# Kernel optimization log

Hardware: AMD Instinct MI355X
Metric: run time of the kernel (lower is better)

The kernel has to match this reference:

```python
import jax, jax.numpy as jnp
import numpy as np

B, S, H = 64, 512, 768        # batch, seq_len, bert hidden
WE, ML, D = 4, 5, 50          # word_enhance_size, max_lexicon_length, word emb dim
V, T = 700000, 21             # lexicon vocab, num_labels


def setup_inputs() -> dict:
    key = jax.random.key(0)
    ks = jax.random.split(key, 10)
    return {
        "sequence_output": jax.random.normal(ks[0], (B, S, H), jnp.float32),
        "soft_lexicon_ids": jax.random.randint(ks[1], (B, S, WE, ML), 0, V),
        "soft_lexicon_weights": jax.random.uniform(ks[2], (B, S, WE, ML), jnp.float32),
        "label_ids": jax.random.randint(ks[3], (B, S), 0, T),
        "attention_mask": jnp.ones((B, S), jnp.int32),
        "word_emb": jax.random.normal(ks[4], (V, D), jnp.float32) * 0.02,
        "W": jax.random.normal(ks[5], (H + WE * D, T), jnp.float32) * 0.02,
        "b": jnp.zeros((T,), jnp.float32),
        "start_trans": jax.random.normal(ks[6], (T,), jnp.float32) * 0.1,
        "end_trans": jax.random.normal(ks[7], (T,), jnp.float32) * 0.1,
        "trans": jax.random.normal(ks[8], (T, T), jnp.float32) * 0.1,
    }


def _crf_nll(emissions, tags, mask, start_trans, end_trans, trans):
    """torchcrf-style CRF negative log-likelihood, reduction='sum'.
    emissions [B,S,T], tags [B,S] int, mask [B,S] in {0,1} (mask[:,0]==1)."""
    maskf = mask.astype(emissions.dtype)
    # ---- numerator: score of the gold path ----
    em_sc = jnp.take_along_axis(emissions, tags[..., None], axis=-1)[..., 0]  # [B,S]
    trans_sc = trans[tags[:, :-1], tags[:, 1:]]                               # [B,S-1]
    num = start_trans[tags[:, 0]] + em_sc[:, 0] \
        + jnp.sum((trans_sc + em_sc[:, 1:]) * maskf[:, 1:], axis=-1)
    last_idx = jnp.sum(mask, axis=-1).astype(jnp.int32) - 1
    last_tags = jnp.take_along_axis(tags, last_idx[:, None], axis=1)[:, 0]
    num = num + end_trans[last_tags]
    # ---- denominator: forward algorithm (logsumexp recursion) ----
    alpha0 = start_trans[None, :] + emissions[:, 0]          # [B,T]
    em_t = jnp.swapaxes(emissions[:, 1:], 0, 1)              # [S-1,B,T]
    mk_t = jnp.swapaxes(mask[:, 1:], 0, 1)                   # [S-1,B]

    def step(alpha, inp):
        e_t, m_t = inp
        nxt = jax.scipy.special.logsumexp(
            alpha[:, :, None] + trans[None, :, :] + e_t[:, None, :], axis=1)
        return jnp.where(m_t[:, None] > 0, nxt, alpha), None

    alpha, _ = jax.lax.scan(step, alpha0, (em_t, mk_t))
    logZ = jax.scipy.special.logsumexp(alpha + end_trans[None, :], axis=-1)
    return -jnp.sum(num - logZ)


def reference(sequence_output, soft_lexicon_ids, soft_lexicon_weights, label_ids,
              attention_mask, word_emb, W, b, start_trans, end_trans, trans):
    Bn, Sn = sequence_output.shape[0], sequence_output.shape[1]
    # soft-lexicon gather + weighted sum over matched words: [B,S,WE,ML,D] -> [B,S,WE,D]
    lex = word_emb[soft_lexicon_ids]                                   # gather
    lex = jnp.einsum('bswld,bswl->bswd', lex, soft_lexicon_weights)    # weight + reduce ML
    lex = lex.reshape(Bn, Sn, -1)                                      # [B,S,WE*D]
    feats = jnp.concatenate([sequence_output, lex], axis=-1)           # [B,S,H+WE*D]
    logits = feats @ W + b                                             # [B,S,T]
    loss = _crf_nll(logits, label_ids, attention_mask, start_trans, end_trans, trans)
    return logits, loss
```

## Files before the change

kernel.cpp:

```cpp
#include <hip/hip_runtime.h>

constexpr int B  = 64, S = 512, H = 768, WE = 4, ML = 5, D = 50, T = 21;
constexpr int NT = B * S;
constexpr int HF = H + WE * D;
constexpr int HP = 1024;
constexpr int TPW = 4;
constexpr float LOG2E = 1.4426950408889634f;
constexpr float LN2   = 0.6931471805599453f;

__global__ void k_wprep(const float* __restrict__ W, float* __restrict__ Wp) {
  int idx = blockIdx.x * 256 + threadIdx.x;
  if (idx < T * HP) {
    int t = idx >> 10;
    int h = idx & (HP - 1);
    Wp[idx] = (h < HF) ? W[h * T + t] : 0.f;
  }
}

__launch_bounds__(256)
__global__ void k_logits(const float* __restrict__ seq,
                         const int*   __restrict__ ids,
                         const float* __restrict__ wts,
                         const float* __restrict__ emb,
                         const float* __restrict__ Wp,
                         const float* __restrict__ bias,
                         float* __restrict__ out) {
  __shared__ __align__(16) float lexs[4][TPW * 200];
  const int wave = threadIdx.x >> 6;
  const int lane = threadIdx.x & 63;
  const int tok0 = (blockIdx.x * 4 + wave) * TPW;

  for (int o = lane; o < TPW * 200; o += 64) {
    int k = o / 200, r = o - k * 200;
    int w = r / 50,  d = r - w * 50;
    int base = ((tok0 + k) * WE + w) * ML;
    float a = 0.f;
#pragma unroll
    for (int l = 0; l < ML; ++l) {
      int   id = ids[base + l];
      float wt = wts[base + l];
      a += wt * emb[(long)id * D + d];
    }
    lexs[wave][o] = a;
  }
  __syncthreads();

  float acc[TPW][T];
#pragma unroll
  for (int k = 0; k < TPW; ++k)
#pragma unroll
    for (int t = 0; t < T; ++t) acc[k][t] = 0.f;

#pragma unroll
  for (int it = 0; it < 4; ++it) {
    const int h0 = it * 256 + lane * 4;
    float4 f[TPW];
#pragma unroll
    for (int k = 0; k < TPW; ++k) {
      if (h0 < H)        f[k] = *(const float4*)&seq[(long)(tok0 + k) * H + h0];
      else if (h0 < HF)  f[k] = *(const float4*)&lexs[wave][k * 200 + (h0 - H)];
      else               f[k] = make_float4(0.f, 0.f, 0.f, 0.f);
    }
#pragma unroll
    for (int t = 0; t < T; ++t) {
      float4 wv = *(const float4*)&Wp[t * HP + h0];
#pragma unroll
      for (int k = 0; k < TPW; ++k) {
        acc[k][t] += f[k].x * wv.x;
        acc[k][t] += f[k].y * wv.y;
        acc[k][t] += f[k].z * wv.z;
        acc[k][t] += f[k].w * wv.w;
      }
    }
  }

#pragma unroll
  for (int k = 0; k < TPW; ++k)
#pragma unroll
    for (int t = 0; t < T; ++t) {
      float v = acc[k][t];
#pragma unroll
      for (int m = 32; m; m >>= 1) v += __shfl_xor(v, m, 64);
      acc[k][t] = v;
    }

  if (lane == 0) {
#pragma unroll
    for (int k = 0; k < TPW; ++k)
#pragma unroll
      for (int t = 0; t < T; ++t)
        out[(long)(tok0 + k) * T + t] = acc[k][t] + bias[t];
  }
}

__global__ void k_crf(const float* __restrict__ logits,
                      const int*   __restrict__ labels,
                      const int*   __restrict__ mask,
                      const float* __restrict__ start_t,
                      const float* __restrict__ end_t,
                      const float* __restrict__ trans,
                      float* __restrict__ part) {
  const int b = blockIdx.x;
  const int lane = threadIdx.x;
  const long base = (long)b * S;
  const int j = lane % 21;
  int p = lane / 21; if (p == 3) p = 0;
  const int i0 = p * 7;

  float tr[7];
#pragma unroll
  for (int ii = 0; ii < 7; ++ii) tr[ii] = trans[(i0 + ii) * T + j];

  float np = 0.f; int cnt = 0;
  for (int s = lane; s < S; s += 64) {
    int tg = labels[base + s];
    int mk = mask[base + s];
    cnt += mk;
    if (s == 0) {
      np += start_t[tg] + logits[base * T + tg];
    } else {
      int tp = labels[base + s - 1];
      np += mk ? (trans[tp * T + tg] + logits[(base + s) * T + tg]) : 0.f;
    }
  }
#pragma unroll
  for (int m = 32; m; m >>= 1) {
    np  += __shfl_xor(np, m, 64);
    cnt += __shfl_xor(cnt, m, 64);
  }
  int last = cnt - 1;
  int lt = labels[base + last];
  float num = np + end_t[lt];

  float a = start_t[j] + logits[base * T + j];
  float e_nxt = logits[(base + 1) * T + j];
  int   m_nxt = mask[base + 1];
  for (int s = 1; s < S; ++s) {
    float e = e_nxt; int mk = m_nxt;
    if (s + 1 < S) {
      e_nxt = logits[(base + s + 1) * T + j];
      m_nxt = mask[base + s + 1];
    }
    float x[7]; float xm = -3e38f;
#pragma unroll
    for (int ii = 0; ii < 7; ++ii) {
      float ai = __shfl(a, i0 + ii, 64);
      x[ii] = ai + tr[ii];
      xm = fmaxf(xm, x[ii]);
    }
    float m1 = __shfl(xm, j, 64);
    float m2 = __shfl(xm, j + 21, 64);
    float m3 = __shfl(xm, j + 42, 64);
    float mm = fmaxf(fmaxf(m1, m2), m3);
    float ss = 0.f;
#pragma unroll
    for (int ii = 0; ii < 7; ++ii) ss += exp2f((x[ii] - mm) * LOG2E);
    float s1 = __shfl(ss, j, 64);
    float s2 = __shfl(ss, j + 21, 64);
    float s3 = __shfl(ss, j + 42, 64);
    float anew = e + mm + LN2 * log2f(s1 + s2 + s3);
    a = mk ? anew : a;
  }

  float y  = (lane < T) ? a + end_t[lane] : -3e38f;
  float ym = y;
#pragma unroll
  for (int m = 32; m; m >>= 1) ym = fmaxf(ym, __shfl_xor(ym, m, 64));
  float z = (lane < T) ? exp2f((y - ym) * LOG2E) : 0.f;
#pragma unroll
  for (int m = 32; m; m >>= 1) z += __shfl_xor(z, m, 64);
  float logZ = ym + LN2 * log2f(z);

  if (lane == 0) part[b] = logZ - num;
}

__global__ void k_loss(const float* __restrict__ part, float* __restrict__ out_loss) {
  int lane = threadIdx.x;
  float v = part[lane];
#pragma unroll
  for (int m = 32; m; m >>= 1) v += __shfl_xor(v, m, 64);
  if (lane == 0) out_loss[0] = v;
}

extern "C" void kernel_launch(void* const* d_in, const int* in_sizes, int n_in,
                              void* d_out, int out_size, void* d_ws, size_t ws_size,
                              hipStream_t stream) {
  const float* seq  = (const float*)d_in[0];
  const int*   ids  = (const int*)  d_in[1];
  const float* wts  = (const float*)d_in[2];
  const int*   lbl  = (const int*)  d_in[3];
  const int*   msk  = (const int*)  d_in[4];
  const float* emb  = (const float*)d_in[5];
  const float* W    = (const float*)d_in[6];
  const float* bias = (const float*)d_in[7];
  const float* st   = (const float*)d_in[8];
  const float* en   = (const float*)d_in[9];
  const float* tr   = (const float*)d_in[10];

  float* out  = (float*)d_out;
  float* Wp   = (float*)d_ws;
  float* part = Wp + T * HP;

  k_wprep <<<(T * HP + 255) / 256, 256, 0, stream>>>(W, Wp);
  k_logits<<<NT / (4 * TPW), 256, 0, stream>>>(seq, ids, wts, emb, Wp, bias, out);
  k_crf   <<<B, 64, 0, stream>>>(out, lbl, msk, st, en, tr, part);
  k_loss  <<<1, 64, 0, stream>>>(part, out + (long)NT * T);
}
```

Before: 616.6 us.

## Halve tokens per wave in logits kernel and restructure CRF recursion in log2 domain

The logits kernel now processes two tokens per wave instead of four and gets an occupancy hint in launch_bounds, so register pressure drops and more waves stay resident. The CRF forward recursion now works in base-2 log space and uses a single shift (alpha of state 0) in place of a max reduction, which removes two shuffle rounds per step. It also loads emissions for three timesteps at once and prefetches four groups ahead. Using alpha[0] as the shift without a true max risks overflow or underflow in exp2 when the alpha values spread widely.

```diff
diff --git a/kernel.cpp b/kernel.cpp
--- a/kernel.cpp
+++ b/kernel.cpp
@@ -4,7 +4,7 @@
 constexpr int NT = B * S;
 constexpr int HF = H + WE * D;
 constexpr int HP = 1024;
-constexpr int TPW = 4;
+constexpr int TPW = 2;
 constexpr float LOG2E = 1.4426950408889634f;
 constexpr float LN2   = 0.6931471805599453f;
 
@@ -17,7 +17,7 @@
   }
 }
 
-__launch_bounds__(256)
+__launch_bounds__(256, 4)
 __global__ void k_logits(const float* __restrict__ seq,
                          const int*   __restrict__ ids,
                          const float* __restrict__ wts,
@@ -45,51 +45,53 @@
   }
   __syncthreads();
 
-  float acc[TPW][T];
-#pragma unroll
-  for (int k = 0; k < TPW; ++k)
-#pragma unroll
-    for (int t = 0; t < T; ++t) acc[k][t] = 0.f;
+  float acc0[T], acc1[T];
+#pragma unroll
+  for (int t = 0; t < T; ++t) { acc0[t] = 0.f; acc1[t] = 0.f; }
 
 #pragma unroll
   for (int it = 0; it < 4; ++it) {
     const int h0 = it * 256 + lane * 4;
-    float4 f[TPW];
-#pragma unroll
-    for (int k = 0; k < TPW; ++k) {
-      if (h0 < H)        f[k] = *(const float4*)&seq[(long)(tok0 + k) * H + h0];
-      else if (h0 < HF)  f[k] = *(const float4*)&lexs[wave][k * 200 + (h0 - H)];
-      else               f[k] = make_float4(0.f, 0.f, 0.f, 0.f);
-    }
+    float4 f0, f1;
+    if (h0 < H) {
+      f0 = *(const float4*)&seq[(long)(tok0 + 0) * H + h0];
+      f1 = *(const float4*)&seq[(long)(tok0 + 1) * H + h0];
+    } else if (h0 < HF) {
+      f0 = *(const float4*)&lexs[wave][0 * 200 + (h0 - H)];
+      f1 = *(const float4*)&lexs[wave][1 * 200 + (h0 - H)];
+    } else {
+      f0 = make_float4(0.f, 0.f, 0.f, 0.f);
+      f1 = f0;
+    }
+#pragma unroll
+    for (int tg = 0; tg < 3; ++tg) {
+#pragma unroll
+      for (int t7 = 0; t7 < 7; ++t7) {
+        const int t = tg * 7 + t7;
+        float4 wv = *(const float4*)&Wp[t * HP + h0];
+        acc0[t] += f0.x * wv.x + f0.y * wv.y + f0.z * wv.z + f0.w * wv.w;
+        acc1[t] += f1.x * wv.x + f1.y * wv.y + f1.z * wv.z + f1.w * wv.w;
+      }
+    }
+  }
+
+#pragma unroll
+  for (int t = 0; t < T; ++t) {
+    float v0 = acc0[t], v1 = acc1[t];
+#pragma unroll
+    for (int m = 32; m; m >>= 1) {
+      v0 += __shfl_xor(v0, m, 64);
+      v1 += __shfl_xor(v1, m, 64);
+    }
+    acc0[t] = v0; acc1[t] = v1;
+  }
+
+  if (lane == 0) {
 #pragma unroll
     for (int t = 0; t < T; ++t) {
-      float4 wv = *(const float4*)&Wp[t * HP + h0];
-#pragma unroll
-      for (int k = 0; k < TPW; ++k) {
-        acc[k][t] += f[k].x * wv.x;
-        acc[k][t] += f[k].y * wv.y;
-        acc[k][t] += f[k].z * wv.z;
-        acc[k][t] += f[k].w * wv.w;
-      }
-    }
-  }
-
-#pragma unroll
-  for (int k = 0; k < TPW; ++k)
-#pragma unroll
-    for (int t = 0; t < T; ++t) {
-      float v = acc[k][t];
-#pragma unroll
-      for (int m = 32; m; m >>= 1) v += __shfl_xor(v, m, 64);
-      acc[k][t] = v;
-    }
-
-  if (lane == 0) {
-#pragma unroll
-    for (int k = 0; k < TPW; ++k)
-#pragma unroll
-      for (int t = 0; t < T; ++t)
-        out[(long)(tok0 + k) * T + t] = acc[k][t] + bias[t];
+      out[(long)(tok0 + 0) * T + t] = acc0[t] + bias[t];
+      out[(long)(tok0 + 1) * T + t] = acc1[t] + bias[t];
+    }
   }
 }
 
@@ -107,9 +109,9 @@
   int p = lane / 21; if (p == 3) p = 0;
   const int i0 = p * 7;
 
-  float tr[7];
-#pragma unroll
-  for (int ii = 0; ii < 7; ++ii) tr[ii] = trans[(i0 + ii) * T + j];
+  float TR[7];
+#pragma unroll
+  for (int ii = 0; ii < 7; ++ii) TR[ii] = trans[(i0 + ii) * T + j] * LOG2E;
 
   float np = 0.f; int cnt = 0;
   for (int s = lane; s < S; s += 64) {
@@ -132,44 +134,65 @@
   int lt = labels[base + last];
   float num = np + end_t[lt];
 
-  float a = start_t[j] + logits[base * T + j];
-  float e_nxt = logits[(base + 1) * T + j];
-  int   m_nxt = mask[base + 1];
-  for (int s = 1; s < S; ++s) {
-    float e = e_nxt; int mk = m_nxt;
-    if (s + 1 < S) {
-      e_nxt = logits[(base + s + 1) * T + j];
-      m_nxt = mask[base + s + 1];
-    }
-    float x[7]; float xm = -3e38f;
-#pragma unroll
-    for (int ii = 0; ii < 7; ++ii) {
-      float ai = __shfl(a, i0 + ii, 64);
-      x[ii] = ai + tr[ii];
-      xm = fmaxf(xm, x[ii]);
-    }
-    float m1 = __shfl(xm, j, 64);
-    float m2 = __shfl(xm, j + 21, 64);
-    float m3 = __shfl(xm, j + 42, 64);
-    float mm = fmaxf(fmaxf(m1, m2), m3);
-    float ss = 0.f;
-#pragma unroll
-    for (int ii = 0; ii < 7; ++ii) ss += exp2f((x[ii] - mm) * LOG2E);
-    float s1 = __shfl(ss, j, 64);
-    float s2 = __shfl(ss, j + 21, 64);
-    float s3 = __shfl(ss, j + 42, 64);
-    float anew = e + mm + LN2 * log2f(s1 + s2 + s3);
-    a = mk ? anew : a;
-  }
-
-  float y  = (lane < T) ? a + end_t[lane] : -3e38f;
+  const int lq = lane / 21;
+  const int lr = lane - 21 * (lq < 3 ? lq : 0);
+  const int lm = lane < 2 ? lane : 2;
+
+#define CRF_LOAD(E, M, c) do {                                   \
+    int _se = 1 + 3 * (c) + lq; if (_se > S - 1) _se = S - 1;    \
+    E = logits[(base + _se) * T + lr];                           \
+    int _sm = 1 + 3 * (c) + lm; if (_sm > S - 1) _sm = S - 1;    \
+    M = mask[base + _sm];                                        \
+  } while (0)
+
+#define CRF_STEP(E, M, c, stp) do {                              \
+    const int _s = 1 + 3 * (c) + (stp);                          \
+    float en = __shfl(E, (stp) * 21 + j, 64);                    \
+    int   mk = __shfl(M, (stp), 64);                             \
+    float sh = __shfl(A, 0, 64);                                 \
+    float p0 = exp2f(__shfl(A, i0 + 0, 64) + (TR[0] - sh));      \
+    float p1 = exp2f(__shfl(A, i0 + 1, 64) + (TR[1] - sh));      \
+    float p2 = exp2f(__shfl(A, i0 + 2, 64) + (TR[2] - sh));      \
+    float p3 = exp2f(__shfl(A, i0 + 3, 64) + (TR[3] - sh));      \
+    float p4 = exp2f(__shfl(A, i0 + 4, 64) + (TR[4] - sh));      \
+    float p5 = exp2f(__shfl(A, i0 + 5, 64) + (TR[5] - sh));      \
+    float p6 = exp2f(__shfl(A, i0 + 6, 64) + (TR[6] - sh));      \
+    float ss = ((p0 + p1) + (p2 + p3)) + ((p4 + p5) + p6);       \
+    float s1 = __shfl(ss, j, 64);                                \
+    float s2 = __shfl(ss, j + 21, 64);                           \
+    float s3 = __shfl(ss, j + 42, 64);                           \
+    float An = fmaf(en, LOG2E, sh) + __log2f((s1 + s2) + s3);    \
+    A = (mk && _s < S) ? An : A;                                 \
+  } while (0)
+
+#define CRF_STEP3(E, M, c) do { CRF_STEP(E, M, c, 0); CRF_STEP(E, M, c, 1); CRF_STEP(E, M, c, 2); } while (0)
+
+  float A = (start_t[j] + logits[base * T + j]) * LOG2E;
+
+  float E0, E1, E2, E3; int M0, M1, M2, M3;
+  CRF_LOAD(E0, M0, 0); CRF_LOAD(E1, M1, 1);
+  CRF_LOAD(E2, M2, 2); CRF_LOAD(E3, M3, 3);
+
+  for (int g = 0; g < 43; ++g) {
+    const int c = 4 * g;
+    CRF_STEP3(E0, M0, c + 0); CRF_LOAD(E0, M0, c + 4);
+    CRF_STEP3(E1, M1, c + 1); CRF_LOAD(E1, M1, c + 5);
+    CRF_STEP3(E2, M2, c + 2); CRF_LOAD(E2, M2, c + 6);
+    CRF_STEP3(E3, M3, c + 3); CRF_LOAD(E3, M3, c + 7);
+  }
+#undef CRF_LOAD
+#undef CRF_STEP
+#undef CRF_STEP3
+
+  float a_ln = A * LN2;
+  float y  = (lane < T) ? a_ln + end_t[lane] : -3e38f;
   float ym = y;
 #pragma unroll
   for (int m = 32; m; m >>= 1) ym = fmaxf(ym, __shfl_xor(ym, m, 64));
   float z = (lane < T) ? exp2f((y - ym) * LOG2E) : 0.f;
 #pragma unroll
   for (int m = 32; m; m >>= 1) z += __shfl_xor(z, m, 64);
-  float logZ = ym + LN2 * log2f(z);
+  float logZ = ym + LN2 * __log2f(z);
 
   if (lane == 0) part[b] = logZ - num;
 }
```

Result: slower. 1.040 ms (+68.6%).
